# Performance work log

Measured on AMD Instinct MI355X. Metric: run time of the kernel, lower is better.

## Reference

```python
import jax, jax.numpy as jnp
import numpy as np

N = 1024
IN_FEATURES = 128
N_HEADS = 8
N_HIDDEN = 16  # out_features // n_heads = 128 // 8
NEG_SLOPE = 0.2


def setup_inputs() -> dict:
    key = jax.random.key(0)
    k1, k2, k3, k4, k5 = jax.random.split(key, 5)
    h = jax.random.normal(k1, (N, IN_FEATURES), dtype=jnp.float32)
    adj_mat = jax.random.randint(k2, (N, N, 1), 0, 2, dtype=jnp.int32)
    s = jax.random.normal(k3, (N, N, 1), dtype=jnp.float32)
    # linear: nn.Linear(in_features, n_hidden*n_heads, bias=False) -> weight [128, 128]
    W = jax.random.normal(k4, (N_HEADS * N_HIDDEN, IN_FEATURES), dtype=jnp.float32) * 0.1
    # attn: nn.Linear(2*n_hidden, 1, bias=False) -> weight [1, 32]; stored flat [32]
    attn_w = jax.random.normal(k5, (2 * N_HIDDEN,), dtype=jnp.float32) * 0.1
    return {"h": h, "adj_mat": adj_mat, "s": s, "W": W, "attn_w": attn_w}


def reference(h, adj_mat, s, W, attn_w):
    n_nodes = h.shape[0]
    # g: [N, heads, hidden]
    g = (h @ W.T).reshape(n_nodes, N_HEADS, N_HIDDEN)
    # attn(cat(g_i, g_j)) = a_src . g_i + a_dst . g_j  (linear decomposes over concat)
    a_src = attn_w[:N_HIDDEN]
    a_dst = attn_w[N_HIDDEN:]
    src = jnp.einsum('ihf,f->ih', g, a_src)  # [N, heads]
    dst = jnp.einsum('jhf,f->jh', g, a_dst)  # [N, heads]
    e = jax.nn.leaky_relu(src[:, None, :] + dst[None, :, :], NEG_SLOPE)  # [N, N, heads]
    mask = adj_mat == 0  # [N, N, 1] broadcasts over heads
    neg_inf = jnp.array(-jnp.inf, dtype=e.dtype)
    e = jnp.where(mask, neg_inf, e)
    s_masked = jnp.where(mask, neg_inf, s)  # [N, N, 1]
    a = jax.nn.softmax(e, axis=1)               # [N, N, heads]
    s_prime = jax.nn.softmax(s_masked, axis=1)  # [N, N, 1]
    # NOTE: original applies a third softmax to (a + s_prime) WITHOUT re-masking,
    # so non-edge entries (value 0) get nonzero weight exp(0)/Z — replicated faithfully.
    new_attention = jax.nn.softmax(a + s_prime, axis=1)  # [N, N, heads]
    # dropout is identity in eval mode
    attn_res = jnp.einsum('ijh,jhf->ihf', new_attention, g)  # [N, heads, hidden]
    return attn_res.reshape(n_nodes, N_HEADS * N_HIDDEN)
```

## Files before the change

kernel.cpp:

```cpp
#include <hip/hip_runtime.h>

#define NNODES 1024
#define NHEADS 8
#define NHID 16
#define DIM 128
#define NEG_SLOPE 0.2f

template<int CTRL>
__device__ __forceinline__ float qbcast(float v) {
    return __int_as_float(__builtin_amdgcn_mov_dpp(__float_as_int(v), CTRL, 0xF, 0xF, true));
}

__global__ __launch_bounds__(256) void proj_kernel(
    const float* __restrict__ h, const float* __restrict__ W,
    const float* __restrict__ attn_w,
    float* __restrict__ g, float* __restrict__ srcv, float* __restrict__ dstv)
{
    const int bi = blockIdx.x & 63;
    const int bh = blockIdx.x >> 6;
    const int i0 = bi << 4;
    const int tid = threadIdx.x;
    __shared__ float4 hs[16][33];
    __shared__ float4 ws[16][33];
    const float4* h4 = (const float4*)h;
    const float4* W4 = (const float4*)W;
    {
        const int t0 = tid, t1 = tid + 256;
        hs[t0 >> 5][t0 & 31] = h4[(size_t)i0 * 32 + t0];
        hs[t1 >> 5][t1 & 31] = h4[(size_t)i0 * 32 + t1];
        ws[t0 >> 5][t0 & 31] = W4[(size_t)(bh * 16) * 32 + t0];
        ws[t1 >> 5][t1 & 31] = W4[(size_t)(bh * 16) * 32 + t1];
    }
    __syncthreads();
    const int il = tid >> 4;
    const int f  = tid & 15;
    float p0 = 0.f, p1 = 0.f, p2 = 0.f, p3 = 0.f;
#pragma unroll
    for (int k = 0; k < 32; k += 4) {
        float4 a, b;
        a = hs[il][k];     b = ws[f][k];
        p0 = fmaf(a.x, b.x, fmaf(a.y, b.y, fmaf(a.z, b.z, fmaf(a.w, b.w, p0))));
        a = hs[il][k + 1]; b = ws[f][k + 1];
        p1 = fmaf(a.x, b.x, fmaf(a.y, b.y, fmaf(a.z, b.z, fmaf(a.w, b.w, p1))));
        a = hs[il][k + 2]; b = ws[f][k + 2];
        p2 = fmaf(a.x, b.x, fmaf(a.y, b.y, fmaf(a.z, b.z, fmaf(a.w, b.w, p2))));
        a = hs[il][k + 3]; b = ws[f][k + 3];
        p3 = fmaf(a.x, b.x, fmaf(a.y, b.y, fmaf(a.z, b.z, fmaf(a.w, b.w, p3))));
    }
    const float acc = (p0 + p1) + (p2 + p3);
    const int i = i0 + il;
    g[(size_t)i * DIM + bh * NHID + f] = acc;
    float sv = acc * attn_w[f];
    float dv = acc * attn_w[NHID + f];
#pragma unroll
    for (int off = 1; off <= 8; off <<= 1) {
        sv += __shfl_xor(sv, off, 64);
        dv += __shfl_xor(dv, off, 64);
    }
    if (f == 0) { srcv[i * NHEADS + bh] = sv; dstv[i * NHEADS + bh] = dv; }
}

__global__ __launch_bounds__(512, 8) void fused_kernel(
    const int* __restrict__ adj, const float* __restrict__ s,
    const float* __restrict__ g, const float* __restrict__ srcv,
    const float* __restrict__ dstv, float* __restrict__ out)
{
    const int i0   = blockIdx.x * 2;
    const int tid  = threadIdx.x;
    const int lane = tid & 63;
    const int wv   = tid >> 6;

    __shared__ float evL[2][NNODES];
    __shared__ float sh_src[2][NHEADS];
    __shared__ float zeA[8][NHEADS][2];
    __shared__ float zsA[8];
    __shared__ float redO[8][2][NHEADS][4][4];
    __shared__ float ztA[8][2][NHEADS];

    const int rA = tid >> 8;
    const int cA = tid & 255;
    float zs;
    {
        const int4   a  = ((const int4*)  adj)[(size_t)(i0 + rA) * (NNODES/4) + cA];
        const float4 sv = ((const float4*)s  )[(size_t)(i0 + rA) * (NNODES/4) + cA];
        float4 e4;
        e4.x = a.x ? __expf(sv.x) : 0.f;
        e4.y = a.y ? __expf(sv.y) : 0.f;
        e4.z = a.z ? __expf(sv.z) : 0.f;
        e4.w = a.w ? __expf(sv.w) : 0.f;
        ((float4*)evL[rA])[cA] = e4;
        zs = (e4.x + e4.y) + (e4.z + e4.w);
    }
    if (tid < 16) sh_src[tid >> 3][tid & 7] =
        srcv[(size_t)(i0 + (tid >> 3)) * NHEADS + (tid & 7)];
#pragma unroll
    for (int off = 1; off <= 32; off <<= 1) zs += __shfl_xor(zs, off, 64);
    if (lane == 0) zsA[wv] = zs;
    __syncthreads();

    const int hA  = tid & 7;
    const int jsA = tid >> 3;
    float ze0 = 0.f, ze1 = 0.f;
    {
        const float sH0 = sh_src[0][hA], sH1 = sh_src[1][hA];
#pragma unroll 2
        for (int t = 0; t < 16; t++) {
            const int j = t * 64 + jsA;
            const float d = dstv[j * NHEADS + hA];
            float e0 = sH0 + d; e0 = e0 > 0.f ? e0 : NEG_SLOPE * e0;
            float e1 = sH1 + d; e1 = e1 > 0.f ? e1 : NEG_SLOPE * e1;
            ze0 += (evL[0][j] != 0.f) ? __expf(e0) : 0.f;
            ze1 += (evL[1][j] != 0.f) ? __expf(e1) : 0.f;
        }
    }
#pragma unroll
    for (int off = 8; off <= 32; off <<= 1) {
        ze0 += __shfl_xor(ze0, off, 64);
        ze1 += __shfl_xor(ze1, off, 64);
    }
    if (lane < NHEADS) { zeA[wv][lane][0] = ze0; zeA[wv][lane][1] = ze1; }
    __syncthreads();

    const int qB  = tid & 3;
    const int hB  = (tid >> 2) & 7;
    const int jsB = tid >> 5;
    float ize[2], izs[2];
    {
        float z0 = 0.f, z1 = 0.f;
#pragma unroll
        for (int w2 = 0; w2 < 8; w2++) { z0 += zeA[w2][hB][0]; z1 += zeA[w2][hB][1]; }
        ize[0] = 1.f / z0; ize[1] = 1.f / z1;
        izs[0] = 1.f / (zsA[0] + zsA[1] + zsA[2] + zsA[3]);
        izs[1] = 1.f / (zsA[4] + zsA[5] + zsA[6] + zsA[7]);
    }
    const float sB0 = sh_src[0][hB], sB1 = sh_src[1][hB];

    float acc0[4] = {0.f,0.f,0.f,0.f};
    float acc1[4] = {0.f,0.f,0.f,0.f};
    float zt0 = 0.f, zt1 = 0.f;
    const float4* g4 = (const float4*)g;
    const int rowb0 = jsB * 4;
    const int fq    = hB * 4 + qB;

#pragma unroll 1
    for (int tg = 0; tg < 16; tg++) {
        const int jw = tg * 64 + rowb0 + qB;
        const float d = dstv[jw * NHEADS + hB];
        float e0 = sB0 + d; e0 = e0 > 0.f ? e0 : NEG_SLOPE * e0;
        float e1 = sB1 + d; e1 = e1 > 0.f ? e1 : NEG_SLOPE * e1;
        const float x0 = __expf(e0), x1 = __expf(e1);
        const float ev0 = evL[0][jw], ev1 = evL[1][jw];
        const float a0 = (ev0 != 0.f) ? fmaf(x0, ize[0], ev0 * izs[0]) : 0.f;
        const float a1 = (ev1 != 0.f) ? fmaf(x1, ize[1], ev1 * izs[1]) : 0.f;
        const float w0 = __expf(a0), w1 = __expf(a1);
        zt0 += w0; zt1 += w1;

#define KSTEP(K, CTRL)                                                        \
        {                                                                     \
            const int j = tg * 64 + rowb0 + (K);                              \
            const float4 gv = g4[(size_t)j * 32 + fq];                        \
            const float wk0 = qbcast<CTRL>(w0);                               \
            const float wk1 = qbcast<CTRL>(w1);                               \
            acc0[0] = fmaf(wk0, gv.x, acc0[0]);                               \
            acc0[1] = fmaf(wk0, gv.y, acc0[1]);                               \
            acc0[2] = fmaf(wk0, gv.z, acc0[2]);                               \
            acc0[3] = fmaf(wk0, gv.w, acc0[3]);                               \
            acc1[0] = fmaf(wk1, gv.x, acc1[0]);                               \
            acc1[1] = fmaf(wk1, gv.y, acc1[1]);                               \
            acc1[2] = fmaf(wk1, gv.z, acc1[2]);                               \
            acc1[3] = fmaf(wk1, gv.w, acc1[3]);                               \
        }
        KSTEP(0, 0x00)
        KSTEP(1, 0x55)
        KSTEP(2, 0xAA)
        KSTEP(3, 0xFF)
#undef KSTEP
    }

#pragma unroll
    for (int m = 0; m < 4; m++) {
        acc0[m] += __shfl_xor(acc0[m], 32, 64);
        acc1[m] += __shfl_xor(acc1[m], 32, 64);
    }
    zt0 += __shfl_xor(zt0, 1, 64); zt0 += __shfl_xor(zt0, 2, 64); zt0 += __shfl_xor(zt0, 32, 64);
    zt1 += __shfl_xor(zt1, 1, 64); zt1 += __shfl_xor(zt1, 2, 64); zt1 += __shfl_xor(zt1, 32, 64);
    if (lane < 32) {
        *(float4*)&redO[wv][0][hB][qB][0] = make_float4(acc0[0], acc0[1], acc0[2], acc0[3]);
        *(float4*)&redO[wv][1][hB][qB][0] = make_float4(acc1[0], acc1[1], acc1[2], acc1[3]);
        if ((lane & 3) == 0) { ztA[wv][0][hB] = zt0; ztA[wv][1][hB] = zt1; }
    }
    __syncthreads();
    if (tid < 256) {
        const int rr = tid >> 7;
        const int hf = tid & 127;
        const int oh = hf >> 4;
        const int qq = (hf >> 2) & 3;
        const int mm = hf & 3;
        float v = 0.f, z = 0.f;
#pragma unroll
        for (int w2 = 0; w2 < 8; w2++) {
            v += redO[w2][rr][oh][qq][mm];
            z += ztA[w2][rr][oh];
        }
        out[(size_t)(i0 + rr) * DIM + hf] = v / z;
    }
}

extern "C" void kernel_launch(void* const* d_in, const int* in_sizes, int n_in,
                              void* d_out, int out_size, void* d_ws, size_t ws_size,
                              hipStream_t stream) {
    const float* h      = (const float*)d_in[0];
    const int*   adj    = (const int*)  d_in[1];
    const float* s      = (const float*)d_in[2];
    const float* W      = (const float*)d_in[3];
    const float* attn_w = (const float*)d_in[4];
    float* out = (float*)d_out;

    float* g    = (float*)d_ws;
    float* srcv = g    + (size_t)NNODES * DIM;
    float* dstv = srcv + (size_t)NNODES * NHEADS;

    proj_kernel <<<512, 256, 0, stream>>>(h, W, attn_w, g, srcv, dstv);
    fused_kernel<<<NNODES / 2, 512, 0, stream>>>(adj, s, g, srcv, dstv, out);
}
```

Measured before the change: 82.37 us.

## Stage dst scores into LDS via async global-to-LDS copies

Each block copies the full dstv array into shared memory using global_load_lds, and both attention passes read it from LDS instead of global memory. Softmax normalizer reciprocals are computed once into shared memory by a few threads, with an extra barrier. Loop unroll factors are raised and the occupancy hint is lowered. This trades redundant per-block loading of 32KB and higher LDS use, which lowers occupancy, for cheaper per-iteration reads. There is also a risk of missing waits on the async copy.

```diff
diff --git a/kernel.cpp b/kernel.cpp
--- a/kernel.cpp
+++ b/kernel.cpp
@@ -9,6 +9,12 @@
 template<int CTRL>
 __device__ __forceinline__ float qbcast(float v) {
     return __int_as_float(__builtin_amdgcn_mov_dpp(__float_as_int(v), CTRL, 0xF, 0xF, true));
+}
+
+__device__ __forceinline__ void async_cp16(const float4* gsrc, float4* ldst) {
+    __builtin_amdgcn_global_load_lds(
+        (const __attribute__((address_space(1))) void*)gsrc,
+        (__attribute__((address_space(3))) void*)ldst, 16, 0, 0);
 }
 
 __global__ __launch_bounds__(256) void proj_kernel(
@@ -60,7 +66,7 @@
     if (f == 0) { srcv[i * NHEADS + bh] = sv; dstv[i * NHEADS + bh] = dv; }
 }
 
-__global__ __launch_bounds__(512, 8) void fused_kernel(
+__global__ __launch_bounds__(512, 4) void fused_kernel(
     const int* __restrict__ adj, const float* __restrict__ s,
     const float* __restrict__ g, const float* __restrict__ srcv,
     const float* __restrict__ dstv, float* __restrict__ out)
@@ -71,12 +77,25 @@
     const int wv   = tid >> 6;
 
     __shared__ float evL[2][NNODES];
+    __shared__ float dstL[NNODES * NHEADS];
     __shared__ float sh_src[2][NHEADS];
     __shared__ float zeA[8][NHEADS][2];
     __shared__ float zsA[8];
+    __shared__ float statE[2][NHEADS];
+    __shared__ float statS[2];
     __shared__ float redO[8][2][NHEADS][4][4];
     __shared__ float ztA[8][2][NHEADS];
 
+    {
+        const float4* dv4 = (const float4*)dstv;
+        float4* dl4 = (float4*)dstL;
+        const int wb = wv << 6;
+#pragma unroll
+        for (int k = 0; k < 4; k++)
+            async_cp16(dv4 + k * 512 + tid, dl4 + k * 512 + wb);
+    }
+    if (tid < 16) sh_src[tid >> 3][tid & 7] =
+        srcv[(size_t)(i0 + (tid >> 3)) * NHEADS + (tid & 7)];
     const int rA = tid >> 8;
     const int cA = tid & 255;
     float zs;
@@ -91,8 +110,6 @@
         ((float4*)evL[rA])[cA] = e4;
         zs = (e4.x + e4.y) + (e4.z + e4.w);
     }
-    if (tid < 16) sh_src[tid >> 3][tid & 7] =
-        srcv[(size_t)(i0 + (tid >> 3)) * NHEADS + (tid & 7)];
 #pragma unroll
     for (int off = 1; off <= 32; off <<= 1) zs += __shfl_xor(zs, off, 64);
     if (lane == 0) zsA[wv] = zs;
@@ -103,10 +120,10 @@
     float ze0 = 0.f, ze1 = 0.f;
     {
         const float sH0 = sh_src[0][hA], sH1 = sh_src[1][hA];
-#pragma unroll 2
+#pragma unroll 4
         for (int t = 0; t < 16; t++) {
             const int j = t * 64 + jsA;
-            const float d = dstv[j * NHEADS + hA];
+            const float d = dstL[j * NHEADS + hA];
             float e0 = sH0 + d; e0 = e0 > 0.f ? e0 : NEG_SLOPE * e0;
             float e1 = sH1 + d; e1 = e1 > 0.f ? e1 : NEG_SLOPE * e1;
             ze0 += (evL[0][j] != 0.f) ? __expf(e0) : 0.f;
@@ -120,20 +137,24 @@
     }
     if (lane < NHEADS) { zeA[wv][lane][0] = ze0; zeA[wv][lane][1] = ze1; }
     __syncthreads();
+    if (tid < 16) {
+        const int hh = tid & 7, rr = tid >> 3;
+        float z = 0.f;
+#pragma unroll
+        for (int w2 = 0; w2 < 8; w2++) z += zeA[w2][hh][rr];
+        statE[rr][hh] = 1.f / z;
+    } else if (tid < 18) {
+        const int rr = tid - 16;
+        statS[rr] = 1.f / (zsA[rr*4] + zsA[rr*4+1] + zsA[rr*4+2] + zsA[rr*4+3]);
+    }
+    __syncthreads();
 
     const int qB  = tid & 3;
     const int hB  = (tid >> 2) & 7;
     const int jsB = tid >> 5;
-    float ize[2], izs[2];
-    {
-        float z0 = 0.f, z1 = 0.f;
-#pragma unroll
-        for (int w2 = 0; w2 < 8; w2++) { z0 += zeA[w2][hB][0]; z1 += zeA[w2][hB][1]; }
-        ize[0] = 1.f / z0; ize[1] = 1.f / z1;
-        izs[0] = 1.f / (zsA[0] + zsA[1] + zsA[2] + zsA[3]);
-        izs[1] = 1.f / (zsA[4] + zsA[5] + zsA[6] + zsA[7]);
-    }
-    const float sB0 = sh_src[0][hB], sB1 = sh_src[1][hB];
+    const float ize0 = statE[0][hB], ize1 = statE[1][hB];
+    const float izs0 = statS[0],     izs1 = statS[1];
+    const float sB0  = sh_src[0][hB], sB1 = sh_src[1][hB];
 
     float acc0[4] = {0.f,0.f,0.f,0.f};
     float acc1[4] = {0.f,0.f,0.f,0.f};
@@ -142,16 +163,16 @@
     const int rowb0 = jsB * 4;
     const int fq    = hB * 4 + qB;
 
-#pragma unroll 1
+#pragma unroll 2
     for (int tg = 0; tg < 16; tg++) {
         const int jw = tg * 64 + rowb0 + qB;
-        const float d = dstv[jw * NHEADS + hB];
+        const float d = dstL[jw * NHEADS + hB];
         float e0 = sB0 + d; e0 = e0 > 0.f ? e0 : NEG_SLOPE * e0;
         float e1 = sB1 + d; e1 = e1 > 0.f ? e1 : NEG_SLOPE * e1;
         const float x0 = __expf(e0), x1 = __expf(e1);
         const float ev0 = evL[0][jw], ev1 = evL[1][jw];
-        const float a0 = (ev0 != 0.f) ? fmaf(x0, ize[0], ev0 * izs[0]) : 0.f;
-        const float a1 = (ev1 != 0.f) ? fmaf(x1, ize[1], ev1 * izs[1]) : 0.f;
+        const float a0 = (ev0 != 0.f) ? fmaf(x0, ize0, ev0 * izs0) : 0.f;
+        const float a1 = (ev1 != 0.f) ? fmaf(x1, ize1, ev1 * izs1) : 0.f;
         const float w0 = __expf(a0), w1 = __expf(a1);
         zt0 += w0; zt1 += w1;
 
```

New measurement: 81.63 us. Within noise of the previous version (-0.9%).
